# Kernel tuning notes

Measured on AMD Instinct MI355X. Metric: run time of the kernel, lower is better.

The kernel has to match this reference:

```python
import math
import jax, jax.numpy as jnp
import numpy as np

B, C, F, W_FRAMES = 1, 8, 1024, 512
H = 16                      # num_heads
D = F // H                  # head dim = 64
ROPE_DIM = D // 2           # 32: only first half of head dim is rotated
EXP = 4                     # ffn expansion
EPS = 1e-5
MAX_FREQ = 10.0             # rotary-embedding-torch default


def frame_norm(x, g, b):
    # LayerNorm over the feature axis (axis=2) of (b, c, F, w)
    mu = jnp.mean(x, axis=2, keepdims=True)
    var = jnp.mean(jnp.square(x - mu), axis=2, keepdims=True)
    xn = (x - mu) * jax.lax.rsqrt(var + EPS)
    return xn * g[None, None, :, None] + b[None, None, :, None]


def mc_linear(x, w_pw):
    # per-channel pointwise linear: out[b,c,f,w] = sum_g W[c,f,g] x[b,c,g,w]
    return jnp.einsum('bcgw,cfg->bcfw', x, w_pw)


def apply_rope(t, freqs_seq):
    # t: (b, c, H, w, d); freqs_seq: (w, rot_dim)
    rot_dim = freqs_seq.shape[-1]
    t_rot, t_pass = t[..., :rot_dim], t[..., rot_dim:]
    cos, sin = jnp.cos(freqs_seq), jnp.sin(freqs_seq)
    x1, x2 = t_rot[..., 0::2], t_rot[..., 1::2]
    rh = jnp.stack([-x2, x1], axis=-1).reshape(t_rot.shape)  # interleaved rotate_half
    return jnp.concatenate([t_rot * cos + rh * sin, t_pass], axis=-1)


def attention(x, w_q, w_o, rope_freqs):
    b, c, f, w = x.shape
    # NOTE: source uses q_proj for q, k AND v (k_proj/v_proj unused)
    p = mc_linear(x, w_q)                                    # (b,c,F,w)
    t = p.transpose(0, 1, 3, 2).reshape(b, c, w, H, D).transpose(0, 1, 3, 2, 4)  # (b,c,H,w,d)
    pos = jnp.arange(w, dtype=t.dtype)
    freqs_seq = jnp.repeat(pos[:, None] * rope_freqs[None, :], 2, axis=-1)  # (w, rot_dim)
    q = apply_rope(t, freqs_seq)
    k = apply_rope(t, freqs_seq)
    v = t
    scores = jnp.einsum('bchqd,bchkd->bchqk', q, k) / math.sqrt(f)  # scaled by sqrt(features)!
    a = jax.nn.softmax(scores, axis=-1)
    o = jnp.einsum('bchqk,bchkd->bchqd', a, v)
    o = o.transpose(0, 1, 3, 2, 4).reshape(b, c, w, f).transpose(0, 1, 3, 2)  # (b,c,F,w)
    return mc_linear(o, w_o)


def setup_inputs() -> dict:
    key = jax.random.key(0)
    ks = jax.random.split(key, 8)
    s = 1.0 / math.sqrt(F)
    se = 1.0 / math.sqrt(F * EXP)
    x = jax.random.normal(ks[0], (B, C, F, W_FRAMES), dtype=jnp.float32)
    w_q = jax.random.uniform(ks[1], (C, F, F), jnp.float32, -s, s)
    w_o = jax.random.uniform(ks[2], (C, F, F), jnp.float32, -s, s)
    w1 = jax.random.uniform(ks[3], (C, F * EXP, F), jnp.float32, -s, s)
    w2 = jax.random.uniform(ks[4], (C, F, F * EXP), jnp.float32, -se, se)
    rope_freqs = jnp.linspace(1.0, MAX_FREQ / 2, ROPE_DIM // 2, dtype=jnp.float32) * math.pi
    return {
        'x': x,
        'norm1_g': jnp.ones((F,), jnp.float32), 'norm1_b': jnp.zeros((F,), jnp.float32),
        'w_q': w_q, 'w_o': w_o, 'rope_freqs': rope_freqs,
        'norm2_g': jnp.ones((F,), jnp.float32), 'norm2_b': jnp.zeros((F,), jnp.float32),
        'w1': w1, 'w2': w2,
    }


def reference(x, norm1_g, norm1_b, w_q, w_o, rope_freqs, norm2_g, norm2_b, w1, w2):
    # FrameTransformerEncoder, eval mode (dropout = identity)
    z = frame_norm(x, norm1_g, norm1_b)
    x = x + attention(z, w_q, w_o, rope_freqs)
    z = frame_norm(x, norm2_g, norm2_b)
    z = mc_linear(jax.nn.gelu(mc_linear(z, w1), approximate=False), w2)
    return x + z
```

## Files before the change

kernel.cpp:

```cpp
#include <hip/hip_runtime.h>
#include <math.h>

#define CC 8
#define FF 1024
#define WW 512
#define HH 16
#define DD 64
#define FE 4096
#define EPS_ 1e-5f

typedef __attribute__((ext_vector_type(8))) short bf16x8;
typedef __attribute__((ext_vector_type(4))) float f32x4;

static __device__ __forceinline__ unsigned short f2bf(float f) {
    unsigned u = __float_as_uint(f);
    u += 0x7fffu + ((u >> 16) & 1u);
    return (unsigned short)(u >> 16);
}
static __device__ __forceinline__ float bf2f(unsigned short h) {
    return __uint_as_float(((unsigned)h) << 16);
}
static __device__ __forceinline__ float gelu_exact(float v) {
    return 0.5f * v * (1.0f + erff(v * 0.70710678118654752f));
}

typedef const __attribute__((address_space(1))) unsigned int* gas_p;
typedef __attribute__((address_space(3))) unsigned int* las_p;
static __device__ __forceinline__ void gload_lds16(const void* g, void* l) {
    __builtin_amdgcn_global_load_lds((gas_p)g, (las_p)l, 16, 0, 0);
}

__global__ __launch_bounds__(256) void fn_stats_k(
    const float* __restrict__ x, float2* __restrict__ part)
{
    int c  = blockIdx.z;
    int w0 = blockIdx.x * 64;
    int f0 = blockIdx.y * 128;
    int t  = threadIdx.x, wl = t & 63, fg = t >> 6;
    const float* xc = x + (size_t)c * FF * WW;

    float s = 0.f, q = 0.f;
    #pragma unroll 8
    for (int i = 0; i < 32; i++) {
        int f = f0 + fg + 4 * i;
        float v = xc[(size_t)f * WW + w0 + wl];
        s += v; q += v * v;
    }
    __shared__ float ss[4][64], sq_[4][64];
    ss[fg][wl] = s; sq_[fg][wl] = q;
    __syncthreads();
    if (fg == 0) {
        float S = 0.f, Q = 0.f;
        #pragma unroll
        for (int j = 0; j < 4; j++) { S += ss[j][wl]; Q += sq_[j][wl]; }
        part[((size_t)c * WW + w0 + wl) * 8 + blockIdx.y] = make_float2(S, Q);
    }
}

__global__ __launch_bounds__(256) void fn_apply_k(
    const float* __restrict__ x, const float2* __restrict__ part,
    const float* __restrict__ g, const float* __restrict__ b,
    unsigned short* __restrict__ zt)
{
    int c  = blockIdx.z;
    int w0 = blockIdx.x * 64;
    int f0 = blockIdx.y * 64;
    int t  = threadIdx.x, wl = t & 63, fg = t >> 6;

    __shared__ float smu[64], srv[64];
    __shared__ float sT[64][65];

    if (t < 64) {
        float S = 0.f, Q = 0.f;
        #pragma unroll
        for (int fs = 0; fs < 8; fs++) {
            float2 v = part[((size_t)c * WW + w0 + t) * 8 + fs];
            S += v.x; Q += v.y;
        }
        float mu  = S * (1.f / FF);
        float var = Q * (1.f / FF) - mu * mu;
        smu[t] = mu;
        srv[t] = rsqrtf(var + EPS_);
    }
    const float* xc = x + (size_t)c * FF * WW;
    #pragma unroll
    for (int i = 0; i < 16; i++) {
        int fl = fg * 16 + i;
        sT[fl][wl] = xc[(size_t)(f0 + fl) * WW + w0 + wl];
    }
    __syncthreads();

    unsigned short* ztc = zt + (size_t)c * WW * FF;
    float gv = g[f0 + wl], bv = b[f0 + wl];
    #pragma unroll
    for (int i = 0; i < 16; i++) {
        int wr = fg * 16 + i;
        ztc[(size_t)(w0 + wr) * FF + f0 + wl] =
            f2bf((sT[wl][wr] - smu[wr]) * srv[wr] * gv + bv);
    }
}

__global__ __launch_bounds__(256, 3) void gemm_v3_k(
    const float* __restrict__ A, const unsigned short* __restrict__ Bt,
    float* __restrict__ Outf, unsigned short* __restrict__ Outb,
    const float* __restrict__ Add, int M, int K, int mode)
{
    int bid = blockIdx.x;
    int c   = bid & 7;
    int rem = bid >> 3;
    int nt  = rem & 3;
    int mt  = rem >> 2;
    int m0  = mt * 64, n0 = nt * 128;
    const float*          Ac = A  + (size_t)c * M * K;
    const unsigned short* Bc = Bt + ((size_t)c * 512 + n0) * K;

    __shared__ unsigned short sA[2][64 * 72];
    __shared__ unsigned short sB[2][128 * 64];

    int t    = threadIdx.x;
    int lane = t & 63;
    int wid  = t >> 6;
    int frl  = lane & 15, fgr = lane >> 4;
    int WM   = (wid >> 1) * 32, WN = (wid & 1) * 64;

    f32x4 acc[2][4];
    #pragma unroll
    for (int i = 0; i < 2; i++)
        #pragma unroll
        for (int j = 0; j < 4; j++) acc[i][j] = (f32x4){0.f, 0.f, 0.f, 0.f};

    int arow = t >> 4;
    int acol = (t & 15) * 4;
    float4 ar[4];

    int bro   = lane >> 3;
    int bslot = (lane & 7) ^ bro;

    auto loadA = [&](int k0) {
        #pragma unroll
        for (int p = 0; p < 4; p++)
            ar[p] = *reinterpret_cast<const float4*>(
                Ac + (size_t)(m0 + p * 16 + arow) * K + k0 + acol);
    };
    auto writeA = [&](int buf) {
        #pragma unroll
        for (int p = 0; p < 4; p++) {
            ushort4 h;
            h.x = f2bf(ar[p].x); h.y = f2bf(ar[p].y);
            h.z = f2bf(ar[p].z); h.w = f2bf(ar[p].w);
            *reinterpret_cast<ushort4*>(&sA[buf][(p * 16 + arow) * 72 + acol]) = h;
        }
    };
    auto stageB = [&](int buf, int k0) {
        #pragma unroll
        for (int r = 0; r < 4; r++) {
            int rbase = wid * 32 + r * 8;
            gload_lds16(Bc + (size_t)(rbase + bro) * K + k0 + bslot * 8,
                        &sB[buf][rbase * 64]);
        }
    };

    loadA(0);
    stageB(0, 0);
    writeA(0);
    __syncthreads();

    int NT = K >> 6;
    for (int kt = 0; kt < NT; ++kt) {
        int cur = kt & 1;
        if (kt + 1 < NT) {
            loadA((kt + 1) << 6);
            stageB(cur ^ 1, (kt + 1) << 6);
        }
        #pragma unroll
        for (int ks = 0; ks < 2; ks++) {
            bf16x8 af[2], bfv[4];
            #pragma unroll
            for (int mi = 0; mi < 2; mi++)
                af[mi] = *reinterpret_cast<const bf16x8*>(
                    &sA[cur][(WM + mi * 16 + frl) * 72 + ks * 32 + fgr * 8]);
            #pragma unroll
            for (int ni = 0; ni < 4; ni++) {
                int row  = WN + ni * 16 + frl;
                int slot = ((ks << 2) | fgr) ^ (frl & 7);
                bfv[ni] = *reinterpret_cast<const bf16x8*>(
                    &sB[cur][row * 64 + slot * 8]);
            }
            #pragma unroll
            for (int mi = 0; mi < 2; mi++)
                #pragma unroll
                for (int ni = 0; ni < 4; ni++)
                    acc[mi][ni] = __builtin_amdgcn_mfma_f32_16x16x32_bf16(
                        af[mi], bfv[ni], acc[mi][ni], 0, 0, 0);
        }
        if (kt + 1 < NT) writeA(cur ^ 1);
        __syncthreads();
    }

    if (mode == 1) {
        #pragma unroll
        for (int mi = 0; mi < 2; mi++)
            #pragma unroll
            for (int ni = 0; ni < 4; ni++) {
                int mrow = m0 + WM + mi * 16 + fgr * 4;
                int ncol = n0 + WN + ni * 16 + frl;
                #pragma unroll
                for (int r = 0; r < 4; r++) {
                    size_t o = ((size_t)c * M + mrow + r) * 512 + ncol;
                    Outf[o] = acc[mi][ni][r] + Add[o];
                }
            }
    } else {
        bool gel = (mode == 2);
        #pragma unroll
        for (int mi = 0; mi < 2; mi++)
            #pragma unroll
            for (int ni = 0; ni < 4; ni++) {
                f32x4 v = acc[mi][ni];
                if (gel) {
                    v[0] = gelu_exact(v[0]); v[1] = gelu_exact(v[1]);
                    v[2] = gelu_exact(v[2]); v[3] = gelu_exact(v[3]);
                }
                int mrow = m0 + WM + mi * 16 + fgr * 4;
                int ncol = n0 + WN + ni * 16 + frl;
                ushort4 h;
                h.x = f2bf(v[0]); h.y = f2bf(v[1]);
                h.z = f2bf(v[2]); h.w = f2bf(v[3]);
                *reinterpret_cast<ushort4*>(
                    &Outb[((size_t)c * 512 + ncol) * M + mrow]) = h;
            }
    }
}

__global__ __launch_bounds__(256) void attn_mfma_k(
    const unsigned short* __restrict__ pt, const float* __restrict__ fr,
    unsigned short* __restrict__ ot)
{
    int ch = blockIdx.y;
    int c  = ch >> 4, h = ch & 15;
    int q0 = blockIdx.x * 64;
    int t  = threadIdx.x;
    int lane = t & 63;
    int wid  = t >> 6;
    int frl  = lane & 15, fgr = lane >> 4;

    const unsigned short* base = pt + (size_t)c * WW * FF + h * DD;

    __shared__ unsigned short Qs[64 * 72];
    __shared__ unsigned short Ks[64 * 72];
    __shared__ unsigned short Vt[64 * 72];
    __shared__ unsigned short Ps[4 * 16 * 72];

    {
        int kr = t >> 3, d0 = (t & 7) * 8;
        #pragma unroll
        for (int r = 0; r < 2; r++) {
            int row = kr + r * 32;
            int w   = q0 + row;
            bf16x8 v = *reinterpret_cast<const bf16x8*>(&base[(size_t)w * FF + d0]);
            bf16x8 o;
            if (d0 < 32) {
                #pragma unroll
                for (int j = 0; j < 8; j += 2) {
                    float x1 = bf2f((unsigned short)v[j]);
                    float x2 = bf2f((unsigned short)v[j + 1]);
                    float sn, cs;
                    __sincosf((float)w * fr[(d0 + j) >> 1], &sn, &cs);
                    o[j]     = (short)f2bf(x1 * cs - x2 * sn);
                    o[j + 1] = (short)f2bf(x2 * cs + x1 * sn);
                }
            } else o = v;
            *reinterpret_cast<bf16x8*>(&Qs[row * 72 + d0]) = o;
        }
    }

    f32x4 oacc[4];
    float m_[4], l_[4];
    #pragma unroll
    for (int i = 0; i < 4; i++) {
        oacc[i] = (f32x4){0.f, 0.f, 0.f, 0.f};
        m_[i] = -1e30f; l_[i] = 0.f;
    }
    unsigned short* myP = &Ps[wid * 16 * 72];
    int wq0 = wid * 16;

    for (int k0 = 0; k0 < WW; k0 += 64) {
        __syncthreads();
        {
            int kr = t >> 3, d0 = (t & 7) * 8;
            #pragma unroll
            for (int r = 0; r < 2; r++) {
                int row = kr + r * 32;
                int w   = k0 + row;
                bf16x8 v = *reinterpret_cast<const bf16x8*>(&base[(size_t)w * FF + d0]);
                bf16x8 o;
                if (d0 < 32) {
                    #pragma unroll
                    for (int j = 0; j < 8; j += 2) {
                        float x1 = bf2f((unsigned short)v[j]);
                        float x2 = bf2f((unsigned short)v[j + 1]);
                        float sn, cs;
                        __sincosf((float)w * fr[(d0 + j) >> 1], &sn, &cs);
                        o[j]     = (short)f2bf(x1 * cs - x2 * sn);
                        o[j + 1] = (short)f2bf(x2 * cs + x1 * sn);
                    }
                } else o = v;
                *reinterpret_cast<bf16x8*>(&Ks[row * 72 + d0]) = o;
            }
        }
        {
            int d  = t & 63;
            int kb = (t >> 6) * 8;
            #pragma unroll
            for (int r = 0; r < 2; r++) {
                int kk = kb + r * 32;
                bf16x8 o;
                #pragma unroll
                for (int j = 0; j < 8; j++)
                    o[j] = (short)base[(size_t)(k0 + kk + j) * FF + d];
                *reinterpret_cast<bf16x8*>(&Vt[d * 72 + kk]) = o;
            }
        }
        __syncthreads();

        f32x4 s[4];
        #pragma unroll
        for (int nt = 0; nt < 4; nt++) s[nt] = (f32x4){0.f, 0.f, 0.f, 0.f};
        bf16x8 aq0 = *reinterpret_cast<const bf16x8*>(&Qs[(wq0 + frl) * 72 + fgr * 8]);
        bf16x8 aq1 = *reinterpret_cast<const bf16x8*>(&Qs[(wq0 + frl) * 72 + 32 + fgr * 8]);
        #pragma unroll
        for (int nt = 0; nt < 4; nt++) {
            bf16x8 b0 = *reinterpret_cast<const bf16x8*>(&Ks[(nt * 16 + frl) * 72 + fgr * 8]);
            bf16x8 b1 = *reinterpret_cast<const bf16x8*>(&Ks[(nt * 16 + frl) * 72 + 32 + fgr * 8]);
            s[nt] = __builtin_amdgcn_mfma_f32_16x16x32_bf16(aq0, b0, s[nt], 0, 0, 0);
            s[nt] = __builtin_amdgcn_mfma_f32_16x16x32_bf16(aq1, b1, s[nt], 0, 0, 0);
        }

        #pragma unroll
        for (int r = 0; r < 4; r++) {
            float sv[4];
            #pragma unroll
            for (int nt = 0; nt < 4; nt++) sv[nt] = s[nt][r] * (1.f / 32.f);
            float mx = fmaxf(fmaxf(sv[0], sv[1]), fmaxf(sv[2], sv[3]));
            mx = fmaxf(mx, __shfl_xor(mx, 1, 64));
            mx = fmaxf(mx, __shfl_xor(mx, 2, 64));
            mx = fmaxf(mx, __shfl_xor(mx, 4, 64));
            mx = fmaxf(mx, __shfl_xor(mx, 8, 64));
            float mn    = fmaxf(m_[r], mx);
            float scale = __expf(m_[r] - mn);
            float rs = 0.f;
            #pragma unroll
            for (int nt = 0; nt < 4; nt++) {
                float p = __expf(sv[nt] - mn);
                myP[(fgr * 4 + r) * 72 + nt * 16 + frl] = f2bf(p);
                rs += p;
            }
            rs += __shfl_xor(rs, 1, 64);
            rs += __shfl_xor(rs, 2, 64);
            rs += __shfl_xor(rs, 4, 64);
            rs += __shfl_xor(rs, 8, 64);
            l_[r] = l_[r] * scale + rs;
            m_[r] = mn;
            #pragma unroll
            for (int dt = 0; dt < 4; dt++) oacc[dt][r] *= scale;
        }

        bf16x8 ap0 = *reinterpret_cast<const bf16x8*>(&myP[frl * 72 + fgr * 8]);
        bf16x8 ap1 = *reinterpret_cast<const bf16x8*>(&myP[frl * 72 + 32 + fgr * 8]);
        #pragma unroll
        for (int dt = 0; dt < 4; dt++) {
            bf16x8 b0 = *reinterpret_cast<const bf16x8*>(&Vt[(dt * 16 + frl) * 72 + fgr * 8]);
            bf16x8 b1 = *reinterpret_cast<const bf16x8*>(&Vt[(dt * 16 + frl) * 72 + 32 + fgr * 8]);
            oacc[dt] = __builtin_amdgcn_mfma_f32_16x16x32_bf16(ap0, b0, oacc[dt], 0, 0, 0);
            oacc[dt] = __builtin_amdgcn_mfma_f32_16x16x32_bf16(ap1, b1, oacc[dt], 0, 0, 0);
        }
    }

    unsigned short* ob = ot + (size_t)c * WW * FF + h * DD;
    #pragma unroll
    for (int r = 0; r < 4; r++) {
        float inv = 1.f / l_[r];
        int w = q0 + wq0 + fgr * 4 + r;
        #pragma unroll
        for (int dt = 0; dt < 4; dt++)
            ob[(size_t)w * FF + dt * 16 + frl] = f2bf(oacc[dt][r] * inv);
    }
}

extern "C" void kernel_launch(void* const* d_in, const int* in_sizes, int n_in,
                              void* d_out, int out_size, void* d_ws, size_t ws_size,
                              hipStream_t stream)
{
    const float* x  = (const float*)d_in[0];
    const float* g1 = (const float*)d_in[1];
    const float* b1 = (const float*)d_in[2];
    const float* wq = (const float*)d_in[3];
    const float* wo = (const float*)d_in[4];
    const float* fr = (const float*)d_in[5];
    const float* g2 = (const float*)d_in[6];
    const float* b2 = (const float*)d_in[7];
    const float* w1 = (const float*)d_in[8];
    const float* w2 = (const float*)d_in[9];

    const size_t SZ = (size_t)CC * FF * WW;
    char* wsb = (char*)d_ws;
    unsigned short* zt  = (unsigned short*)(wsb);
    unsigned short* ptb = (unsigned short*)(wsb + 2 * SZ);
    unsigned short* otb = (unsigned short*)(wsb + 4 * SZ);
    float*          x2  = (float*)        (wsb + 6 * SZ);
    unsigned short* h1t = (unsigned short*)(wsb + 10 * SZ);
    float2*         prt = (float2*)       (wsb + 18 * SZ);

    dim3 b256(256);
    dim3 gst(WW / 64, FF / 128, CC);
    dim3 gap(WW / 64, FF / 64, CC);

    fn_stats_k<<<gst, b256, 0, stream>>>(x, prt);
    fn_apply_k<<<gap, b256, 0, stream>>>(x, prt, g1, b1, zt);
    gemm_v3_k<<<dim3(8 * 4 * (FF / 64)), b256, 0, stream>>>(
        wq, zt, nullptr, ptb, nullptr, FF, FF, 0);
    attn_mfma_k<<<dim3(WW / 64, CC * HH), b256, 0, stream>>>(ptb, fr, otb);
    gemm_v3_k<<<dim3(8 * 4 * (FF / 64)), b256, 0, stream>>>(
        wo, otb, x2, nullptr, x, FF, FF, 1);
    fn_stats_k<<<gst, b256, 0, stream>>>(x2, prt);
    fn_apply_k<<<gap, b256, 0, stream>>>(x2, prt, g2, b2, zt);
    gemm_v3_k<<<dim3(8 * 4 * (FE / 64)), b256, 0, stream>>>(
        w1, zt, nullptr, h1t, nullptr, FE, FF, 2);
    gemm_v3_k<<<dim3(8 * 4 * (FF / 64)), b256, 0, stream>>>(
        w2, h1t, (float*)d_out, nullptr, x2, FF, FE, 1);
}
```

Measured before the change: 282.8 us.

## Add 128x128-tile specialized GEMM kernel for the W1 expansion layer with fused GELU

Adds a dedicated GEMM kernel for the FFN up-projection (W1) that uses 128x128 output tiles per block, with each wave computing a 64x64 sub-tile, instead of the generic 64-row tile kernel. It double-buffers LDS, converts the fp32 weights to bf16 while staging them, loads B asynchronously with a swizzled layout, and applies exact GELU in the epilogue. The larger tile is meant to raise arithmetic intensity and cut redundant weight and activation loads for the largest GEMM. The cost is more registers per thread (64 accumulator floats plus 8 float4 prefetch registers) and fewer blocks in the grid.

```diff
diff --git a/kernel.cpp b/kernel.cpp
--- a/kernel.cpp
+++ b/kernel.cpp
@@ -230,6 +230,119 @@
                     &Outb[((size_t)c * 512 + ncol) * M + mrow]) = h;
             }
     }
+}
+
+__global__ __launch_bounds__(256, 2) void gemm_w1_k(
+    const float* __restrict__ A, const unsigned short* __restrict__ Bt,
+    unsigned short* __restrict__ Outb, int M, int K)
+{
+    int bid = blockIdx.x;
+    int c   = bid & 7;
+    int rem = bid >> 3;
+    int nt  = rem & 3;
+    int mt  = rem >> 2;
+    int m0  = mt * 128, n0 = nt * 128;
+    const float*          Ac = A  + (size_t)c * M * K;
+    const unsigned short* Bc = Bt + ((size_t)c * 512 + n0) * K;
+
+    __shared__ unsigned short sA[2][128 * 72];
+    __shared__ unsigned short sB[2][128 * 64];
+
+    int t    = threadIdx.x;
+    int lane = t & 63;
+    int wid  = t >> 6;
+    int frl  = lane & 15, fgr = lane >> 4;
+    int WM   = (wid >> 1) * 64, WN = (wid & 1) * 64;
+
+    f32x4 acc[4][4];
+    #pragma unroll
+    for (int i = 0; i < 4; i++)
+        #pragma unroll
+        for (int j = 0; j < 4; j++) acc[i][j] = (f32x4){0.f, 0.f, 0.f, 0.f};
+
+    int arow = t >> 4;
+    int acol = (t & 15) * 4;
+    float4 ar[8];
+
+    int bro   = lane >> 3;
+    int bslot = (lane & 7) ^ bro;
+
+    auto loadA = [&](int k0) {
+        #pragma unroll
+        for (int p = 0; p < 8; p++)
+            ar[p] = *reinterpret_cast<const float4*>(
+                Ac + (size_t)(m0 + p * 16 + arow) * K + k0 + acol);
+    };
+    auto writeA = [&](int buf) {
+        #pragma unroll
+        for (int p = 0; p < 8; p++) {
+            ushort4 h;
+            h.x = f2bf(ar[p].x); h.y = f2bf(ar[p].y);
+            h.z = f2bf(ar[p].z); h.w = f2bf(ar[p].w);
+            *reinterpret_cast<ushort4*>(&sA[buf][(p * 16 + arow) * 72 + acol]) = h;
+        }
+    };
+    auto stageB = [&](int buf, int k0) {
+        #pragma unroll
+        for (int r = 0; r < 4; r++) {
+            int rbase = wid * 32 + r * 8;
+            gload_lds16(Bc + (size_t)(rbase + bro) * K + k0 + bslot * 8,
+                        &sB[buf][rbase * 64]);
+        }
+    };
+
+    loadA(0);
+    stageB(0, 0);
+    writeA(0);
+    __syncthreads();
+
+    int NT = K >> 6;
+    for (int kt = 0; kt < NT; ++kt) {
+        int cur = kt & 1;
+        if (kt + 1 < NT) {
+            loadA((kt + 1) << 6);
+            stageB(cur ^ 1, (kt + 1) << 6);
+        }
+        #pragma unroll
+        for (int ks = 0; ks < 2; ks++) {
+            bf16x8 af[4], bfv[4];
+            #pragma unroll
+            for (int mi = 0; mi < 4; mi++)
+                af[mi] = *reinterpret_cast<const bf16x8*>(
+                    &sA[cur][(WM + mi * 16 + frl) * 72 + ks * 32 + fgr * 8]);
+            #pragma unroll
+            for (int ni = 0; ni < 4; ni++) {
+                int row  = WN + ni * 16 + frl;
+                int slot = ((ks << 2) | fgr) ^ (frl & 7);
+                bfv[ni] = *reinterpret_cast<const bf16x8*>(
+                    &sB[cur][row * 64 + slot * 8]);
+            }
+            #pragma unroll
+            for (int mi = 0; mi < 4; mi++)
+                #pragma unroll
+                for (int ni = 0; ni < 4; ni++)
+                    acc[mi][ni] = __builtin_amdgcn_mfma_f32_16x16x32_bf16(
+                        af[mi], bfv[ni], acc[mi][ni], 0, 0, 0);
+        }
+        if (kt + 1 < NT) writeA(cur ^ 1);
+        __syncthreads();
+    }
+
+    #pragma unroll
+    for (int mi = 0; mi < 4; mi++)
+        #pragma unroll
+        for (int ni = 0; ni < 4; ni++) {
+            f32x4 v = acc[mi][ni];
+            v[0] = gelu_exact(v[0]); v[1] = gelu_exact(v[1]);
+            v[2] = gelu_exact(v[2]); v[3] = gelu_exact(v[3]);
+            int mrow = m0 + WM + mi * 16 + fgr * 4;
+            int ncol = n0 + WN + ni * 16 + frl;
+            ushort4 h;
+            h.x = f2bf(v[0]); h.y = f2bf(v[1]);
+            h.z = f2bf(v[2]); h.w = f2bf(v[3]);
+            *reinterpret_cast<ushort4*>(
+                &Outb[((size_t)c * 512 + ncol) * M + mrow]) = h;
+        }
 }
 
 __global__ __launch_bounds__(256) void attn_mfma_k(
@@ -424,8 +537,8 @@
         wo, otb, x2, nullptr, x, FF, FF, 1);
     fn_stats_k<<<gst, b256, 0, stream>>>(x2, prt);
     fn_apply_k<<<gap, b256, 0, stream>>>(x2, prt, g2, b2, zt);
-    gemm_v3_k<<<dim3(8 * 4 * (FE / 64)), b256, 0, stream>>>(
-        w1, zt, nullptr, h1t, nullptr, FE, FF, 2);
+    gemm_w1_k<<<dim3(8 * 4 * (FE / 128)), b256, 0, stream>>>(
+        w1, zt, h1t, FE, FF);
     gemm_v3_k<<<dim3(8 * 4 * (FF / 64)), b256, 0, stream>>>(
         w2, h1t, (float*)d_out, nullptr, x2, FF, FE, 1);
 }
```

After: 277.4 us. About the same (-1.9%).

## Load fp32 weight fragments directly into registers, drop A shared-memory staging

Applied to the files above, without the earlier changes.

The GEMM kernel no longer stages the fp32 weight operand through LDS. Each wave loads its own MFMA A-fragments straight from global memory into registers and converts them with the packed v_cvt_pk_bf16_f32 instruction, which removes the LDS writes and reads for A and frees LDS for higher occupancy. The M tile becomes a template parameter: 128 rows for the wide FFN1 GEMM, with occupancy hints adjusted per instantiation. The risk is less coalesced global loads for A (each lane reads 32-byte row chunks) and more register pressure from the larger fragment arrays.

```diff
diff --git a/kernel.cpp b/kernel.cpp
--- a/kernel.cpp
+++ b/kernel.cpp
@@ -11,6 +11,7 @@
 
 typedef __attribute__((ext_vector_type(8))) short bf16x8;
 typedef __attribute__((ext_vector_type(4))) float f32x4;
+typedef __attribute__((ext_vector_type(4))) unsigned u32x4;
 
 static __device__ __forceinline__ unsigned short f2bf(float f) {
     unsigned u = __float_as_uint(f);
@@ -22,6 +23,11 @@
 }
 static __device__ __forceinline__ float gelu_exact(float v) {
     return 0.5f * v * (1.0f + erff(v * 0.70710678118654752f));
+}
+static __device__ __forceinline__ unsigned cvt_pk_bf16(float lo, float hi) {
+    unsigned r;
+    asm("v_cvt_pk_bf16_f32 %0, %1, %2" : "=v"(r) : "v"(lo), "v"(hi));
+    return r;
 }
 
 typedef const __attribute__((address_space(1))) unsigned int* gas_p;
@@ -100,57 +106,67 @@
     }
 }
 
-__global__ __launch_bounds__(256, 3) void gemm_v3_k(
+template<int BMF, int MINW>
+__global__ __launch_bounds__(256, MINW) void gemm_v5_k(
     const float* __restrict__ A, const unsigned short* __restrict__ Bt,
     float* __restrict__ Outf, unsigned short* __restrict__ Outb,
     const float* __restrict__ Add, int M, int K, int mode)
 {
+    constexpr int BM = BMF * 32;
     int bid = blockIdx.x;
     int c   = bid & 7;
     int rem = bid >> 3;
     int nt  = rem & 3;
     int mt  = rem >> 2;
-    int m0  = mt * 64, n0 = nt * 128;
+    int m0  = mt * BM, n0 = nt * 128;
     const float*          Ac = A  + (size_t)c * M * K;
     const unsigned short* Bc = Bt + ((size_t)c * 512 + n0) * K;
 
-    __shared__ unsigned short sA[2][64 * 72];
     __shared__ unsigned short sB[2][128 * 64];
 
     int t    = threadIdx.x;
     int lane = t & 63;
     int wid  = t >> 6;
     int frl  = lane & 15, fgr = lane >> 4;
-    int WM   = (wid >> 1) * 32, WN = (wid & 1) * 64;
-
-    f32x4 acc[2][4];
+    int wm   = (wid >> 1) * (BMF * 16);
+    int wn   = (wid & 1) * 64;
+
+    f32x4 acc[BMF][4];
     #pragma unroll
-    for (int i = 0; i < 2; i++)
+    for (int i = 0; i < BMF; i++)
         #pragma unroll
         for (int j = 0; j < 4; j++) acc[i][j] = (f32x4){0.f, 0.f, 0.f, 0.f};
 
-    int arow = t >> 4;
-    int acol = (t & 15) * 4;
-    float4 ar[4];
+    float4 ar[BMF][2][2];
+    bf16x8 af[BMF][2];
+    const float* Aw = Ac + (size_t)(m0 + wm + frl) * K + fgr * 8;
+
+    auto loadA = [&](int k0) {
+        #pragma unroll
+        for (int mi = 0; mi < BMF; mi++)
+            #pragma unroll
+            for (int ks = 0; ks < 2; ks++) {
+                const float* p = Aw + (size_t)(mi * 16) * K + k0 + ks * 32;
+                ar[mi][ks][0] = *reinterpret_cast<const float4*>(p);
+                ar[mi][ks][1] = *reinterpret_cast<const float4*>(p + 4);
+            }
+    };
+    auto convertA = [&]() {
+        #pragma unroll
+        for (int mi = 0; mi < BMF; mi++)
+            #pragma unroll
+            for (int ks = 0; ks < 2; ks++) {
+                u32x4 u;
+                u[0] = cvt_pk_bf16(ar[mi][ks][0].x, ar[mi][ks][0].y);
+                u[1] = cvt_pk_bf16(ar[mi][ks][0].z, ar[mi][ks][0].w);
+                u[2] = cvt_pk_bf16(ar[mi][ks][1].x, ar[mi][ks][1].y);
+                u[3] = cvt_pk_bf16(ar[mi][ks][1].z, ar[mi][ks][1].w);
+                af[mi][ks] = *reinterpret_cast<bf16x8*>(&u);
+            }
+    };
 
     int bro   = lane >> 3;
     int bslot = (lane & 7) ^ bro;
-
-    auto loadA = [&](int k0) {
-        #pragma unroll
-        for (int p = 0; p < 4; p++)
-            ar[p] = *reinterpret_cast<const float4*>(
-                Ac + (size_t)(m0 + p * 16 + arow) * K + k0 + acol);
-    };
-    auto writeA = [&](int buf) {
-        #pragma unroll
-        for (int p = 0; p < 4; p++) {
-            ushort4 h;
-            h.x = f2bf(ar[p].x); h.y = f2bf(ar[p].y);
-            h.z = f2bf(ar[p].z); h.w = f2bf(ar[p].w);
-            *reinterpret_cast<ushort4*>(&sA[buf][(p * 16 + arow) * 72 + acol]) = h;
-        }
-    };
     auto stageB = [&](int buf, int k0) {
         #pragma unroll
         for (int r = 0; r < 4; r++) {
@@ -161,8 +177,8 @@
     };
 
     loadA(0);
+    convertA();
     stageB(0, 0);
-    writeA(0);
     __syncthreads();
 
     int NT = K >> 6;
@@ -174,36 +190,32 @@
         }
         #pragma unroll
         for (int ks = 0; ks < 2; ks++) {
-            bf16x8 af[2], bfv[4];
-            #pragma unroll
-            for (int mi = 0; mi < 2; mi++)
-                af[mi] = *reinterpret_cast<const bf16x8*>(
-                    &sA[cur][(WM + mi * 16 + frl) * 72 + ks * 32 + fgr * 8]);
+            bf16x8 bfv[4];
             #pragma unroll
             for (int ni = 0; ni < 4; ni++) {
-                int row  = WN + ni * 16 + frl;
+                int row  = wn + ni * 16 + frl;
                 int slot = ((ks << 2) | fgr) ^ (frl & 7);
                 bfv[ni] = *reinterpret_cast<const bf16x8*>(
                     &sB[cur][row * 64 + slot * 8]);
             }
             #pragma unroll
-            for (int mi = 0; mi < 2; mi++)
+            for (int mi = 0; mi < BMF; mi++)
                 #pragma unroll
                 for (int ni = 0; ni < 4; ni++)
                     acc[mi][ni] = __builtin_amdgcn_mfma_f32_16x16x32_bf16(
-                        af[mi], bfv[ni], acc[mi][ni], 0, 0, 0);
-        }
-        if (kt + 1 < NT) writeA(cur ^ 1);
+                        af[mi][ks], bfv[ni], acc[mi][ni], 0, 0, 0);
+        }
+        if (kt + 1 < NT) convertA();
         __syncthreads();
     }
 
     if (mode == 1) {
         #pragma unroll
-        for (int mi = 0; mi < 2; mi++)
+        for (int mi = 0; mi < BMF; mi++)
             #pragma unroll
             for (int ni = 0; ni < 4; ni++) {
-                int mrow = m0 + WM + mi * 16 + fgr * 4;
-                int ncol = n0 + WN + ni * 16 + frl;
+                int mrow = m0 + wm + mi * 16 + fgr * 4;
+                int ncol = n0 + wn + ni * 16 + frl;
                 #pragma unroll
                 for (int r = 0; r < 4; r++) {
                     size_t o = ((size_t)c * M + mrow + r) * 512 + ncol;
@@ -213,7 +225,7 @@
     } else {
         bool gel = (mode == 2);
         #pragma unroll
-        for (int mi = 0; mi < 2; mi++)
+        for (int mi = 0; mi < BMF; mi++)
             #pragma unroll
             for (int ni = 0; ni < 4; ni++) {
                 f32x4 v = acc[mi][ni];
@@ -221,8 +233,8 @@
                     v[0] = gelu_exact(v[0]); v[1] = gelu_exact(v[1]);
                     v[2] = gelu_exact(v[2]); v[3] = gelu_exact(v[3]);
                 }
-                int mrow = m0 + WM + mi * 16 + fgr * 4;
-                int ncol = n0 + WN + ni * 16 + frl;
+                int mrow = m0 + wm + mi * 16 + fgr * 4;
+                int ncol = n0 + wn + ni * 16 + frl;
                 ushort4 h;
                 h.x = f2bf(v[0]); h.y = f2bf(v[1]);
                 h.z = f2bf(v[2]); h.w = f2bf(v[3]);
@@ -417,15 +429,15 @@
 
     fn_stats_k<<<gst, b256, 0, stream>>>(x, prt);
     fn_apply_k<<<gap, b256, 0, stream>>>(x, prt, g1, b1, zt);
-    gemm_v3_k<<<dim3(8 * 4 * (FF / 64)), b256, 0, stream>>>(
+    gemm_v5_k<2, 4><<<dim3(512), b256, 0, stream>>>(
         wq, zt, nullptr, ptb, nullptr, FF, FF, 0);
     attn_mfma_k<<<dim3(WW / 64, CC * HH), b256, 0, stream>>>(ptb, fr, otb);
-    gemm_v3_k<<<dim3(8 * 4 * (FF / 64)), b256, 0, stream>>>(
+    gemm_v5_k<2, 4><<<dim3(512), b256, 0, stream>>>(
         wo, otb, x2, nullptr, x, FF, FF, 1);
     fn_stats_k<<<gst, b256, 0, stream>>>(x2, prt);
     fn_apply_k<<<gap, b256, 0, stream>>>(x2, prt, g2, b2, zt);
-    gemm_v3_k<<<dim3(8 * 4 * (FE / 64)), b256, 0, stream>>>(
+    gemm_v5_k<4, 2><<<dim3(1024), b256, 0, stream>>>(
         w1, zt, nullptr, h1t, nullptr, FE, FF, 2);
-    gemm_v3_k<<<dim3(8 * 4 * (FF / 64)), b256, 0, stream>>>(
+    gemm_v5_k<2, 4><<<dim3(512), b256, 0, stream>>>(
         w2, h1t, (float*)d_out, nullptr, x2, FF, FE, 1);
 }
```

Result: slower. 484.4 us (+71.3%).

## Template GEMM on tile height, hand-schedule waits, use packed bf16 convert

Applied to the files above, without the earlier changes.

The GEMM kernel is templated on the M tile size, so the large FFN up-projection uses 128-row tiles while the others keep 64. The per-iteration __syncthreads is replaced by explicit vmcnt/lgkmcnt waits plus a raw s_barrier, so the next A tile's global loads stay in flight across the barrier and the MFMA work. The f32-to-bf16 conversion of A now uses the hardware packed v_cvt_pk_bf16_f32 instruction instead of software rounding. The hand-written vmcnt counts depend on the exact number of outstanding loads, so a miscount could cause races. The larger tile also raises register pressure and lowers occupancy for the w1 GEMM.

```diff
diff --git a/kernel.cpp b/kernel.cpp
--- a/kernel.cpp
+++ b/kernel.cpp
@@ -22,6 +22,11 @@
 }
 static __device__ __forceinline__ float gelu_exact(float v) {
     return 0.5f * v * (1.0f + erff(v * 0.70710678118654752f));
+}
+static __device__ __forceinline__ unsigned cvt_pk_bf16(float lo, float hi) {
+    unsigned r;
+    asm("v_cvt_pk_bf16_f32 %0, %1, %2" : "=v"(r) : "v"(lo), "v"(hi));
+    return r;
 }
 
 typedef const __attribute__((address_space(1))) unsigned int* gas_p;
@@ -100,55 +105,61 @@
     }
 }
 
-__global__ __launch_bounds__(256, 3) void gemm_v3_k(
+template<int BM, int MINW>
+__global__ __launch_bounds__(256, MINW) void gemm_v6_k(
     const float* __restrict__ A, const unsigned short* __restrict__ Bt,
     float* __restrict__ Outf, unsigned short* __restrict__ Outb,
     const float* __restrict__ Add, int M, int K, int mode)
 {
+    constexpr int L  = BM / 16;
+    constexpr int MI = BM / 32;
+    constexpr int AP = 72;
+
     int bid = blockIdx.x;
     int c   = bid & 7;
     int rem = bid >> 3;
     int nt  = rem & 3;
     int mt  = rem >> 2;
-    int m0  = mt * 64, n0 = nt * 128;
+    int m0  = mt * BM, n0 = nt * 128;
     const float*          Ac = A  + (size_t)c * M * K;
     const unsigned short* Bc = Bt + ((size_t)c * 512 + n0) * K;
 
-    __shared__ unsigned short sA[2][64 * 72];
+    __shared__ unsigned short sA[2][BM * AP];
     __shared__ unsigned short sB[2][128 * 64];
 
     int t    = threadIdx.x;
     int lane = t & 63;
     int wid  = t >> 6;
     int frl  = lane & 15, fgr = lane >> 4;
-    int WM   = (wid >> 1) * 32, WN = (wid & 1) * 64;
-
-    f32x4 acc[2][4];
+    int WM   = (wid >> 1) * (MI * 16);
+    int WN   = (wid & 1) * 64;
+
+    f32x4 acc[MI][4];
     #pragma unroll
-    for (int i = 0; i < 2; i++)
+    for (int i = 0; i < MI; i++)
         #pragma unroll
         for (int j = 0; j < 4; j++) acc[i][j] = (f32x4){0.f, 0.f, 0.f, 0.f};
 
     int arow = t >> 4;
     int acol = (t & 15) * 4;
-    float4 ar[4];
+    float4 ar[L];
 
     int bro   = lane >> 3;
     int bslot = (lane & 7) ^ bro;
 
     auto loadA = [&](int k0) {
         #pragma unroll
-        for (int p = 0; p < 4; p++)
+        for (int p = 0; p < L; p++)
             ar[p] = *reinterpret_cast<const float4*>(
                 Ac + (size_t)(m0 + p * 16 + arow) * K + k0 + acol);
     };
-    auto writeA = [&](int buf) {
-        #pragma unroll
-        for (int p = 0; p < 4; p++) {
-            ushort4 h;
-            h.x = f2bf(ar[p].x); h.y = f2bf(ar[p].y);
-            h.z = f2bf(ar[p].z); h.w = f2bf(ar[p].w);
-            *reinterpret_cast<ushort4*>(&sA[buf][(p * 16 + arow) * 72 + acol]) = h;
+    auto cvtWriteA = [&](int buf) {
+        #pragma unroll
+        for (int p = 0; p < L; p++) {
+            uint2 u;
+            u.x = cvt_pk_bf16(ar[p].x, ar[p].y);
+            u.y = cvt_pk_bf16(ar[p].z, ar[p].w);
+            *reinterpret_cast<uint2*>(&sA[buf][(p * 16 + arow) * AP + acol]) = u;
         }
     };
     auto stageB = [&](int buf, int k0) {
@@ -161,24 +172,37 @@
     };
 
     loadA(0);
+    asm volatile("s_waitcnt vmcnt(0)" ::: "memory");
+    cvtWriteA(0);
     stageB(0, 0);
-    writeA(0);
-    __syncthreads();
 
     int NT = K >> 6;
     for (int kt = 0; kt < NT; ++kt) {
-        int cur = kt & 1;
-        if (kt + 1 < NT) {
-            loadA((kt + 1) << 6);
-            stageB(cur ^ 1, (kt + 1) << 6);
-        }
+        int  cur  = kt & 1;
+        bool more = (kt + 1 < NT);
+
+        if (more) loadA((kt + 1) << 6);
+        if (more) {
+            if constexpr (BM == 128)
+                asm volatile("s_waitcnt vmcnt(8)" ::: "memory");
+            else
+                asm volatile("s_waitcnt vmcnt(4)" ::: "memory");
+        } else {
+            asm volatile("s_waitcnt vmcnt(0)" ::: "memory");
+        }
+        asm volatile("s_waitcnt lgkmcnt(0)" ::: "memory");
+        __builtin_amdgcn_sched_barrier(0);
+        __builtin_amdgcn_s_barrier();
+
+        if (more) stageB(cur ^ 1, (kt + 1) << 6);
+
         #pragma unroll
         for (int ks = 0; ks < 2; ks++) {
-            bf16x8 af[2], bfv[4];
-            #pragma unroll
-            for (int mi = 0; mi < 2; mi++)
+            bf16x8 af[MI], bfv[4];
+            #pragma unroll
+            for (int mi = 0; mi < MI; mi++)
                 af[mi] = *reinterpret_cast<const bf16x8*>(
-                    &sA[cur][(WM + mi * 16 + frl) * 72 + ks * 32 + fgr * 8]);
+                    &sA[cur][(WM + mi * 16 + frl) * AP + ks * 32 + fgr * 8]);
             #pragma unroll
             for (int ni = 0; ni < 4; ni++) {
                 int row  = WN + ni * 16 + frl;
@@ -187,19 +211,23 @@
                     &sB[cur][row * 64 + slot * 8]);
             }
             #pragma unroll
-            for (int mi = 0; mi < 2; mi++)
+            for (int mi = 0; mi < MI; mi++)
                 #pragma unroll
                 for (int ni = 0; ni < 4; ni++)
                     acc[mi][ni] = __builtin_amdgcn_mfma_f32_16x16x32_bf16(
                         af[mi], bfv[ni], acc[mi][ni], 0, 0, 0);
         }
-        if (kt + 1 < NT) writeA(cur ^ 1);
-        __syncthreads();
+
+        if (more) {
+            asm volatile("s_waitcnt vmcnt(4)" ::: "memory");
+            __builtin_amdgcn_sched_barrier(0);
+            cvtWriteA(cur ^ 1);
+        }
     }
 
     if (mode == 1) {
         #pragma unroll
-        for (int mi = 0; mi < 2; mi++)
+        for (int mi = 0; mi < MI; mi++)
             #pragma unroll
             for (int ni = 0; ni < 4; ni++) {
                 int mrow = m0 + WM + mi * 16 + fgr * 4;
@@ -213,7 +241,7 @@
     } else {
         bool gel = (mode == 2);
         #pragma unroll
-        for (int mi = 0; mi < 2; mi++)
+        for (int mi = 0; mi < MI; mi++)
             #pragma unroll
             for (int ni = 0; ni < 4; ni++) {
                 f32x4 v = acc[mi][ni];
@@ -417,15 +445,15 @@
 
     fn_stats_k<<<gst, b256, 0, stream>>>(x, prt);
     fn_apply_k<<<gap, b256, 0, stream>>>(x, prt, g1, b1, zt);
-    gemm_v3_k<<<dim3(8 * 4 * (FF / 64)), b256, 0, stream>>>(
+    gemm_v6_k<64, 3><<<dim3(512), b256, 0, stream>>>(
         wq, zt, nullptr, ptb, nullptr, FF, FF, 0);
     attn_mfma_k<<<dim3(WW / 64, CC * HH), b256, 0, stream>>>(ptb, fr, otb);
-    gemm_v3_k<<<dim3(8 * 4 * (FF / 64)), b256, 0, stream>>>(
+    gemm_v6_k<64, 3><<<dim3(512), b256, 0, stream>>>(
         wo, otb, x2, nullptr, x, FF, FF, 1);
     fn_stats_k<<<gst, b256, 0, stream>>>(x2, prt);
     fn_apply_k<<<gap, b256, 0, stream>>>(x2, prt, g2, b2, zt);
-    gemm_v3_k<<<dim3(8 * 4 * (FE / 64)), b256, 0, stream>>>(
+    gemm_v6_k<128, 2><<<dim3(1024), b256, 0, stream>>>(
         w1, zt, nullptr, h1t, nullptr, FE, FF, 2);
-    gemm_v3_k<<<dim3(8 * 4 * (FF / 64)), b256, 0, stream>>>(
+    gemm_v6_k<64, 3><<<dim3(512), b256, 0, stream>>>(
         w2, h1t, (float*)d_out, nullptr, x2, FF, FE, 1);
 }
```

Measured after the change: 265.1 us. 1.07x faster.
